# Performance work log

Measured on AMD Instinct MI355X. Metric: run time of the kernel, lower is better.

The kernel has to match this reference:

```python
import jax, jax.numpy as jnp
import numpy as np


def conv_block(x, w1, b1, w2, b2):
    # 1x1 convs == per-pixel channel matmuls. x: [b, C, H, W]
    h = jax.nn.relu(jnp.einsum('bchw,oc->bohw', x, w1) + b1[None, :, None, None])
    return jnp.einsum('bchw,oc->bohw', h, w2) + b2[None, :, None, None]


def setup_inputs() -> dict:
    key = jax.random.key(0)
    ks = jax.random.split(key, 9)
    C, Ck = 256, 256 // 8
    bs, H, W = 4, 64, 64
    s_in = 1.0 / np.sqrt(C)
    s_k = 1.0 / np.sqrt(Ck)
    F_input = jax.random.normal(ks[0], (bs, C, H, W), dtype=jnp.float32)
    return {
        'F_input': F_input,
        'w1a': jax.random.normal(ks[1], (Ck, C), dtype=jnp.float32) * s_in,
        'b1a': jax.random.normal(ks[2], (Ck,), dtype=jnp.float32) * s_in,
        'w1b': jax.random.normal(ks[3], (Ck, Ck), dtype=jnp.float32) * s_k,
        'b1b': jax.random.normal(ks[4], (Ck,), dtype=jnp.float32) * s_k,
        'w2a': jax.random.normal(ks[5], (Ck, C), dtype=jnp.float32) * s_in,
        'b2a': jax.random.normal(ks[6], (Ck,), dtype=jnp.float32) * s_in,
        'w2b': jax.random.normal(ks[7], (Ck, Ck), dtype=jnp.float32) * s_k,
        'b2b': jax.random.normal(ks[8], (Ck,), dtype=jnp.float32) * s_k,
    }


def reference(F_input, w1a, b1a, w1b, b1b, w2a, b2a, w2b, b2b):
    bs, C, H, W = F_input.shape
    N = H * W
    q = conv_block(F_input, w1a, b1a, w1b, b1b).reshape(bs, -1, N)  # [b, Ck, N]
    k = conv_block(F_input, w2a, b2a, w2b, b2b).reshape(bs, -1, N)  # [b, Ck, N]
    # mm_1[b, n, m] = sum_c q[b, c, n] * k[b, c, m]
    scores = jnp.einsum('bcn,bcm->bnm', q, k)  # [b, N, N]
    S = jax.nn.softmax(scores, axis=-1)
    Fr = F_input.reshape(bs, C, N)
    # bmm(F_reshape, S^T): out[b, c, n] = sum_m F[b, c, m] * S[b, n, m]
    mm2 = jnp.einsum('bcm,bnm->bcn', Fr, S).reshape(bs, C, H, W)
    return F_input + mm2
```

## Files before the change

### kernel.cpp

```cpp
#include <hip/hip_runtime.h>
#include <math.h>

typedef __attribute__((ext_vector_type(4))) float f32x4;
typedef __attribute__((ext_vector_type(8))) short bf16x8;
typedef __attribute__((ext_vector_type(4))) unsigned int uint4v;

#define LOG2E 1.4426950408889634f

static __device__ __forceinline__ unsigned short f2bf(float f) {
  union { float f; unsigned int i; } u; u.f = f;
  unsigned int r = u.i + 0x7fffu + ((u.i >> 16) & 1u);
  return (unsigned short)(r >> 16);
}

__global__ __launch_bounds__(256) void k_wprep(const float* __restrict__ w1a,
                                               const float* __restrict__ w2a,
                                               float* __restrict__ w1aT,
                                               float* __restrict__ w2aT) {
  int i = blockIdx.x * 256 + threadIdx.x;
  if (i < 32 * 256) {
    int o = i >> 8, c = i & 255;
    w1aT[c * 32 + o] = w1a[i];
    w2aT[c * 32 + o] = w2a[i];
  }
}

__global__ __launch_bounds__(256) void k_qk(
    const float* __restrict__ F,
    const float* __restrict__ w1aT, const float* __restrict__ b1a,
    const float* __restrict__ w1b,  const float* __restrict__ b1b,
    const float* __restrict__ w2aT, const float* __restrict__ b2a,
    const float* __restrict__ w2b,  const float* __restrict__ b2b,
    unsigned short* __restrict__ Fbf,
    unsigned short* __restrict__ qT,
    unsigned short* __restrict__ kT) {
  const int p = blockIdx.x >> 6;
  const int nflat = ((blockIdx.x & 63) << 8) | threadIdx.x;
  const int b = nflat >> 12, n = nflat & 4095;
  const float* __restrict__ wA = p ? w2aT : w1aT;
  const float* __restrict__ bA = p ? b2a : b1a;
  const float* __restrict__ wB = p ? w2b : w1b;
  const float* __restrict__ bB = p ? b2b : b1b;
  const float* Fb = F + ((size_t)b * 256) * 4096 + n;

  float h[32];
#pragma unroll
  for (int o = 0; o < 32; ++o) h[o] = 0.f;

  for (int c = 0; c < 256; ++c) {
    float f = Fb[(size_t)c * 4096];
    if (p == 0) Fbf[((size_t)b * 256 + c) * 4096 + n] = f2bf(f);
#pragma unroll
    for (int o = 0; o < 32; ++o) h[o] += wA[c * 32 + o] * f;
  }
#pragma unroll
  for (int o = 0; o < 32; ++o) h[o] = fmaxf(h[o] + bA[o], 0.f);

  unsigned int pack[16];
#pragma unroll
  for (int o2 = 0; o2 < 32; o2 += 2) {
    float s0 = bB[o2], s1 = bB[o2 + 1];
#pragma unroll
    for (int o = 0; o < 32; ++o) {
      s0 += wB[o2 * 32 + o] * h[o];
      s1 += wB[(o2 + 1) * 32 + o] * h[o];
    }
    if (p == 0) { s0 *= LOG2E; s1 *= LOG2E; }
    pack[o2 >> 1] = (unsigned int)f2bf(s0) | ((unsigned int)f2bf(s1) << 16);
  }
  unsigned short* dst = (p ? kT : qT) + (size_t)nflat * 32;
  uint4v* d4 = (uint4v*)dst;
#pragma unroll
  for (int i = 0; i < 4; ++i) {
    uint4v v = {pack[4 * i], pack[4 * i + 1], pack[4 * i + 2], pack[4 * i + 3]};
    d4[i] = v;
  }
}

__global__ __launch_bounds__(256, 1) void k_attn(
    const unsigned short* __restrict__ qT,
    const unsigned short* __restrict__ kT,
    const unsigned short* __restrict__ Fbf,
    const float* __restrict__ F,
    float* __restrict__ out) {
  __shared__ unsigned short Vt[256][72];
  __shared__ unsigned short Pb[4][16][72];

  const int tid = threadIdx.x;
  const int w = tid >> 6;
  const int lane = tid & 63;
  const int lo = lane & 15;
  const int hi = lane >> 4;

  const int bid = (int)blockIdx.x;
  const int swz = (bid & 7) * 32 + (bid >> 3);
  const int b = swz >> 6;
  const int n0 = (swz & 63) << 6;
  const int nw = n0 + (w << 4);

  const bf16x8 qfrag =
      *(const bf16x8*)(qT + ((size_t)(b << 12) + nw + lo) * 32 + hi * 8);
  const unsigned short* kTb = kT + ((size_t)(b << 12)) * 32;
  const unsigned short* Fb = Fbf + ((size_t)b << 20);

  f32x4 oacc[16];
#pragma unroll
  for (int i = 0; i < 16; ++i) oacc[i] = (f32x4){0.f, 0.f, 0.f, 0.f};
  float m2[4] = {-INFINITY, -INFINITY, -INFINITY, -INFINITY};
  float lr[4] = {0.f, 0.f, 0.f, 0.f};

  const int c0 = tid >> 3;
  const int ch = tid & 7;

  for (int mt = 0; mt < 64; ++mt) {
    {
      const unsigned short* src = Fb + (size_t)c0 * 4096 + (mt << 6) + (ch << 3);
#pragma unroll
      for (int pp = 0; pp < 8; ++pp) {
        bf16x8 v = *(const bf16x8*)(src + (size_t)(pp * 32) * 4096);
        *(bf16x8*)(&Vt[c0 + pp * 32][ch << 3]) = v;
      }
    }
    __syncthreads();

    f32x4 s[4];
#pragma unroll
    for (int mf = 0; mf < 4; ++mf) {
      bf16x8 kf = *(const bf16x8*)(kTb +
          ((size_t)((mt << 6) + (mf << 4) + lo)) * 32 + hi * 8);
      f32x4 z = (f32x4){0.f, 0.f, 0.f, 0.f};
      s[mf] = __builtin_amdgcn_mfma_f32_16x16x32_bf16(qfrag, kf, z, 0, 0, 0);
    }

    float scale[4];
#pragma unroll
    for (int r = 0; r < 4; ++r) {
      float t = fmaxf(fmaxf(s[0][r], s[1][r]), fmaxf(s[2][r], s[3][r]));
      t = fmaxf(t, __shfl_xor(t, 1));
      t = fmaxf(t, __shfl_xor(t, 2));
      t = fmaxf(t, __shfl_xor(t, 4));
      t = fmaxf(t, __shfl_xor(t, 8));
      float mnew = fmaxf(m2[r], t);
      scale[r] = exp2f(m2[r] - mnew);
      m2[r] = mnew;
    }

    float rsum[4] = {0.f, 0.f, 0.f, 0.f};
#pragma unroll
    for (int mf = 0; mf < 4; ++mf) {
#pragma unroll
      for (int r = 0; r < 4; ++r) {
        float p = exp2f(s[mf][r] - m2[r]);
        rsum[r] += p;
        Pb[w][(hi << 2) + r][(mf << 4) + lo] = f2bf(p);
      }
    }
#pragma unroll
    for (int r = 0; r < 4; ++r) {
      float t = rsum[r];
      t += __shfl_xor(t, 1);
      t += __shfl_xor(t, 2);
      t += __shfl_xor(t, 4);
      t += __shfl_xor(t, 8);
      lr[r] = lr[r] * scale[r] + t;
    }
#pragma unroll
    for (int cs = 0; cs < 16; ++cs) {
#pragma unroll
      for (int r = 0; r < 4; ++r) oacc[cs][r] *= scale[r];
    }

#pragma unroll
    for (int ms = 0; ms < 2; ++ms) {
      bf16x8 pf = *(const bf16x8*)(&Pb[w][lo][(ms << 5) + (hi << 3)]);
#pragma unroll
      for (int cs = 0; cs < 16; ++cs) {
        bf16x8 vf = *(const bf16x8*)(&Vt[(cs << 4) + lo][(ms << 5) + (hi << 3)]);
        oacc[cs] = __builtin_amdgcn_mfma_f32_16x16x32_bf16(pf, vf, oacc[cs], 0, 0, 0);
      }
    }
    __syncthreads();
  }

  float inv[4];
#pragma unroll
  for (int r = 0; r < 4; ++r) inv[r] = 1.f / lr[r];
#pragma unroll
  for (int cs = 0; cs < 16; ++cs) {
#pragma unroll
    for (int r = 0; r < 4; ++r) {
      size_t idx = ((size_t)(b * 256) + (cs << 4) + lo) * 4096 + nw + (hi << 2) + r;
      out[idx] = F[idx] + oacc[cs][r] * inv[r];
    }
  }
}

extern "C" void kernel_launch(void* const* d_in, const int* in_sizes, int n_in,
                              void* d_out, int out_size, void* d_ws, size_t ws_size,
                              hipStream_t stream) {
  const float* F   = (const float*)d_in[0];
  const float* w1a = (const float*)d_in[1];
  const float* b1a = (const float*)d_in[2];
  const float* w1b = (const float*)d_in[3];
  const float* b1b = (const float*)d_in[4];
  const float* w2a = (const float*)d_in[5];
  const float* b2a = (const float*)d_in[6];
  const float* w2b = (const float*)d_in[7];
  const float* b2b = (const float*)d_in[8];
  float* out = (float*)d_out;

  char* ws = (char*)d_ws;
  float* w1aT = (float*)(ws);
  float* w2aT = (float*)(ws + 32768);
  unsigned short* Fbf = (unsigned short*)(ws + 65536);
  unsigned short* qT  = (unsigned short*)(ws + 65536 + 8388608);
  unsigned short* kT  = (unsigned short*)(ws + 65536 + 8388608 + 1048576);

  hipLaunchKernelGGL(k_wprep, dim3(32), dim3(256), 0, stream, w1a, w2a, w1aT, w2aT);
  hipLaunchKernelGGL(k_qk, dim3(128), dim3(256), 0, stream,
                     F, w1aT, b1a, w1b, b1b, w2aT, b2a, w2b, b2b, Fbf, qT, kT);
  hipLaunchKernelGGL(k_attn, dim3(256), dim3(256), 0, stream, qT, kT, Fbf, F, out);
}
```

Baseline: 338.7 us.

## Pipeline attention with async LDS loads, split bf16 convert, rebalance QK kernel

The attention kernel is restructured. It now uses 32-key tiles and triple-buffered V tiles loaded with global_load_lds direct-to-LDS copies, plus XOR-swizzled LDS layouts. Each wave now owns 64 output channels for all 64 queries, with scale factors shared through LDS and rescaling skipped when every scale is 1. The bf16 conversion of F moves into its own vectorized kernel, and the QK projection kernel uses 128-thread blocks, twice the grid and register double-buffered F loads. The output epilogue uses vectorized float4 loads and stores. These changes aim to hide global latency and improve MFMA utilization, at the cost of an extra launch, more barriers per tile and higher LDS use.

```diff
diff --git a/kernel.cpp b/kernel.cpp
--- a/kernel.cpp
+++ b/kernel.cpp
@@ -3,14 +3,27 @@
 
 typedef __attribute__((ext_vector_type(4))) float f32x4;
 typedef __attribute__((ext_vector_type(8))) short bf16x8;
+typedef __attribute__((ext_vector_type(2))) unsigned int uint2v;
 typedef __attribute__((ext_vector_type(4))) unsigned int uint4v;
 
 #define LOG2E 1.4426950408889634f
+#define MT 32
+#define NIT 128
 
 static __device__ __forceinline__ unsigned short f2bf(float f) {
   union { float f; unsigned int i; } u; u.f = f;
   unsigned int r = u.i + 0x7fffu + ((u.i >> 16) & 1u);
   return (unsigned short)(r >> 16);
+}
+
+typedef __attribute__((address_space(3))) unsigned int lds_u32;
+typedef __attribute__((address_space(1))) unsigned int g_u32;
+
+static __device__ __forceinline__ void gload_lds16(const unsigned short* g,
+                                                   const unsigned short* l) {
+  __builtin_amdgcn_global_load_lds(
+      (const g_u32*)(unsigned long long)g,
+      (lds_u32*)(unsigned int)(unsigned long long)l, 16, 0, 0);
 }
 
 __global__ __launch_bounds__(256) void k_wprep(const float* __restrict__ w1a,
@@ -25,33 +38,59 @@
   }
 }
 
-__global__ __launch_bounds__(256) void k_qk(
+__global__ __launch_bounds__(256) void k_cvt(const float* __restrict__ F,
+                                             unsigned short* __restrict__ Fbf) {
+  size_t i = ((size_t)blockIdx.x * 256 + threadIdx.x) * 8;
+  f32x4 a = *(const f32x4*)(F + i);
+  f32x4 b = *(const f32x4*)(F + i + 4);
+  unsigned int u0 = (unsigned int)f2bf(a[0]) | ((unsigned int)f2bf(a[1]) << 16);
+  unsigned int u1 = (unsigned int)f2bf(a[2]) | ((unsigned int)f2bf(a[3]) << 16);
+  unsigned int u2 = (unsigned int)f2bf(b[0]) | ((unsigned int)f2bf(b[1]) << 16);
+  unsigned int u3 = (unsigned int)f2bf(b[2]) | ((unsigned int)f2bf(b[3]) << 16);
+  uint4v v = {u0, u1, u2, u3};
+  *(uint4v*)(Fbf + i) = v;
+}
+
+__global__ __launch_bounds__(128) void k_qk(
     const float* __restrict__ F,
     const float* __restrict__ w1aT, const float* __restrict__ b1a,
     const float* __restrict__ w1b,  const float* __restrict__ b1b,
     const float* __restrict__ w2aT, const float* __restrict__ b2a,
     const float* __restrict__ w2b,  const float* __restrict__ b2b,
-    unsigned short* __restrict__ Fbf,
     unsigned short* __restrict__ qT,
     unsigned short* __restrict__ kT) {
-  const int p = blockIdx.x >> 6;
-  const int nflat = ((blockIdx.x & 63) << 8) | threadIdx.x;
+  const int p = blockIdx.x & 1;
+  const int nflat = (blockIdx.x >> 1) * 128 + threadIdx.x;
   const int b = nflat >> 12, n = nflat & 4095;
-  const float* __restrict__ wA = p ? w2aT : w1aT;
-  const float* __restrict__ bA = p ? b2a : b1a;
-  const float* __restrict__ wB = p ? w2b : w1b;
-  const float* __restrict__ bB = p ? b2b : b1b;
-  const float* Fb = F + ((size_t)b * 256) * 4096 + n;
+  const float* wA = p ? w2aT : w1aT;
+  const float* bA = p ? b2a : b1a;
+  const float* wB = p ? w2b : w1b;
+  const float* bB = p ? b2b : b1b;
+  const float* Fp = F + ((size_t)b * 256) * 4096 + n;
 
   float h[32];
 #pragma unroll
   for (int o = 0; o < 32; ++o) h[o] = 0.f;
 
-  for (int c = 0; c < 256; ++c) {
-    float f = Fb[(size_t)c * 4096];
-    if (p == 0) Fbf[((size_t)b * 256 + c) * 4096 + n] = f2bf(f);
-#pragma unroll
-    for (int o = 0; o < 32; ++o) h[o] += wA[c * 32 + o] * f;
+  float fa[8], fb[8];
+#pragma unroll
+  for (int j = 0; j < 8; ++j) fa[j] = Fp[(size_t)j * 4096];
+
+  for (int cc = 0; cc < 256; cc += 16) {
+#pragma unroll
+    for (int j = 0; j < 8; ++j) fb[j] = Fp[(size_t)(cc + 8 + j) * 4096];
+#pragma unroll
+    for (int j = 0; j < 8; ++j)
+#pragma unroll
+      for (int o = 0; o < 32; ++o) h[o] += wA[(cc + j) * 32 + o] * fa[j];
+    if (cc + 16 < 256) {
+#pragma unroll
+      for (int j = 0; j < 8; ++j) fa[j] = Fp[(size_t)(cc + 16 + j) * 4096];
+    }
+#pragma unroll
+    for (int j = 0; j < 8; ++j)
+#pragma unroll
+      for (int o = 0; o < 32; ++o) h[o] += wA[(cc + 8 + j) * 32 + o] * fb[j];
   }
 #pragma unroll
   for (int o = 0; o < 32; ++o) h[o] = fmaxf(h[o] + bA[o], 0.f);
@@ -83,8 +122,10 @@
     const unsigned short* __restrict__ Fbf,
     const float* __restrict__ F,
     float* __restrict__ out) {
-  __shared__ unsigned short Vt[256][72];
-  __shared__ unsigned short Pb[4][16][72];
+  __shared__ unsigned short Vt[3][256 * MT];
+  __shared__ unsigned short Pb[2][64 * MT];
+  __shared__ float scl[2][64];
+  __shared__ float linv[64];
 
   const int tid = threadIdx.x;
   const int w = tid >> 6;
@@ -96,103 +137,133 @@
   const int swz = (bid & 7) * 32 + (bid >> 3);
   const int b = swz >> 6;
   const int n0 = (swz & 63) << 6;
-  const int nw = n0 + (w << 4);
-
-  const bf16x8 qfrag =
-      *(const bf16x8*)(qT + ((size_t)(b << 12) + nw + lo) * 32 + hi * 8);
+
+  const bf16x8 qfrag = *(const bf16x8*)(
+      qT + ((size_t)(b << 12) + n0 + (w << 4) + lo) * 32 + (hi << 3));
   const unsigned short* kTb = kT + ((size_t)(b << 12)) * 32;
   const unsigned short* Fb = Fbf + ((size_t)b << 20);
 
-  f32x4 oacc[16];
-#pragma unroll
-  for (int i = 0; i < 16; ++i) oacc[i] = (f32x4){0.f, 0.f, 0.f, 0.f};
-  float m2[4] = {-INFINITY, -INFINITY, -INFINITY, -INFINITY};
-  float lr[4] = {0.f, 0.f, 0.f, 0.f};
-
-  const int c0 = tid >> 3;
-  const int ch = tid & 7;
-
-  for (int mt = 0; mt < 64; ++mt) {
+  const int crow = lane >> 2;
+  const int pch = lane & 3;
+
+  f32x4 acc[4][4];
+#pragma unroll
+  for (int i = 0; i < 4; ++i)
+#pragma unroll
+    for (int j = 0; j < 4; ++j) acc[i][j] = (f32x4){0.f, 0.f, 0.f, 0.f};
+  float mrun = -INFINITY, lrun = 0.f;
+
+#pragma unroll
+  for (int i = 0; i < 4; ++i) {
+    int c = i * 64 + (w << 4) + crow;
+    gload_lds16(Fb + (size_t)c * 4096 + ((pch ^ (c & 3)) << 3),
+                &Vt[0][(i * 64 + (w << 4)) * MT]);
+  }
+  bf16x8 kc0 = *(const bf16x8*)(kTb + ((size_t)lo) * 32 + (hi << 3));
+  bf16x8 kc1 = *(const bf16x8*)(kTb + ((size_t)(16 + lo)) * 32 + (hi << 3));
+
+  int vb = 0, vn = 1;
+  for (int t = 0; t < NIT; ++t) {
+    if (t + 1 < NIT) {
+#pragma unroll
+      for (int i = 0; i < 4; ++i) {
+        int c = i * 64 + (w << 4) + crow;
+        gload_lds16(Fb + (size_t)c * 4096 + (size_t)(t + 1) * MT + ((pch ^ (c & 3)) << 3),
+                    &Vt[vn][(i * 64 + (w << 4)) * MT]);
+      }
+    }
+    bf16x8 kn0, kn1;
+    if (t + 1 < NIT) {
+      kn0 = *(const bf16x8*)(kTb + ((size_t)((t + 1) * MT) + lo) * 32 + (hi << 3));
+      kn1 = *(const bf16x8*)(kTb + ((size_t)((t + 1) * MT) + 16 + lo) * 32 + (hi << 3));
+    }
+    f32x4 z = (f32x4){0.f, 0.f, 0.f, 0.f};
+    f32x4 s0 = __builtin_amdgcn_mfma_f32_16x16x32_bf16(kc0, qfrag, z, 0, 0, 0);
+    f32x4 s1 = __builtin_amdgcn_mfma_f32_16x16x32_bf16(kc1, qfrag, z, 0, 0, 0);
+
+    float tmax = fmaxf(fmaxf(fmaxf(s0[0], s0[1]), fmaxf(s0[2], s0[3])),
+                       fmaxf(fmaxf(s1[0], s1[1]), fmaxf(s1[2], s1[3])));
+    tmax = fmaxf(tmax, __shfl_xor(tmax, 16));
+    tmax = fmaxf(tmax, __shfl_xor(tmax, 32));
+    float mnew = fmaxf(mrun, tmax);
+    float sc = exp2f(mrun - mnew);
+    mrun = mnew;
+    float p00 = exp2f(s0[0] - mnew), p01 = exp2f(s0[1] - mnew);
+    float p02 = exp2f(s0[2] - mnew), p03 = exp2f(s0[3] - mnew);
+    float p10 = exp2f(s1[0] - mnew), p11 = exp2f(s1[1] - mnew);
+    float p12 = exp2f(s1[2] - mnew), p13 = exp2f(s1[3] - mnew);
+    float rsum = p00 + p01 + p02 + p03 + p10 + p11 + p12 + p13;
+    rsum += __shfl_xor(rsum, 16);
+    rsum += __shfl_xor(rsum, 32);
+    lrun = lrun * sc + rsum;
+    if (hi == 0) scl[t & 1][(w << 4) + lo] = sc;
+
     {
-      const unsigned short* src = Fb + (size_t)c0 * 4096 + (mt << 6) + (ch << 3);
-#pragma unroll
-      for (int pp = 0; pp < 8; ++pp) {
-        bf16x8 v = *(const bf16x8*)(src + (size_t)(pp * 32) * 4096);
-        *(bf16x8*)(&Vt[c0 + pp * 32][ch << 3]) = v;
+      const int qr = (w << 4) + lo;
+      unsigned short* base = &Pb[t & 1][qr * MT];
+      int ch0 = (hi >> 1), ch1 = 2 + (hi >> 1);
+      uint2v v0 = {(unsigned int)f2bf(p00) | ((unsigned int)f2bf(p01) << 16),
+                   (unsigned int)f2bf(p02) | ((unsigned int)f2bf(p03) << 16)};
+      uint2v v1 = {(unsigned int)f2bf(p10) | ((unsigned int)f2bf(p11) << 16),
+                   (unsigned int)f2bf(p12) | ((unsigned int)f2bf(p13) << 16)};
+      *(uint2v*)(base + (((ch0 ^ (qr & 3)) << 3) | ((hi & 1) << 2))) = v0;
+      *(uint2v*)(base + (((ch1 ^ (qr & 3)) << 3) | ((hi & 1) << 2))) = v1;
+    }
+
+    __syncthreads();
+
+    {
+      f32x4 sv[4];
+      bool one = true;
+#pragma unroll
+      for (int qf = 0; qf < 4; ++qf) {
+        sv[qf] = *(const f32x4*)&scl[t & 1][(qf << 4) + (hi << 2)];
+        one = one && (sv[qf][0] == 1.f) && (sv[qf][1] == 1.f) &&
+              (sv[qf][2] == 1.f) && (sv[qf][3] == 1.f);
       }
-    }
-    __syncthreads();
-
-    f32x4 s[4];
-#pragma unroll
-    for (int mf = 0; mf < 4; ++mf) {
-      bf16x8 kf = *(const bf16x8*)(kTb +
-          ((size_t)((mt << 6) + (mf << 4) + lo)) * 32 + hi * 8);
-      f32x4 z = (f32x4){0.f, 0.f, 0.f, 0.f};
-      s[mf] = __builtin_amdgcn_mfma_f32_16x16x32_bf16(qfrag, kf, z, 0, 0, 0);
-    }
-
-    float scale[4];
-#pragma unroll
-    for (int r = 0; r < 4; ++r) {
-      float t = fmaxf(fmaxf(s[0][r], s[1][r]), fmaxf(s[2][r], s[3][r]));
-      t = fmaxf(t, __shfl_xor(t, 1));
-      t = fmaxf(t, __shfl_xor(t, 2));
-      t = fmaxf(t, __shfl_xor(t, 4));
-      t = fmaxf(t, __shfl_xor(t, 8));
-      float mnew = fmaxf(m2[r], t);
-      scale[r] = exp2f(m2[r] - mnew);
-      m2[r] = mnew;
-    }
-
-    float rsum[4] = {0.f, 0.f, 0.f, 0.f};
-#pragma unroll
-    for (int mf = 0; mf < 4; ++mf) {
-#pragma unroll
-      for (int r = 0; r < 4; ++r) {
-        float p = exp2f(s[mf][r] - m2[r]);
-        rsum[r] += p;
-        Pb[w][(hi << 2) + r][(mf << 4) + lo] = f2bf(p);
+      if (!__all(one)) {
+#pragma unroll
+        for (int qf = 0; qf < 4; ++qf)
+#pragma unroll
+          for (int cs = 0; cs < 4; ++cs) acc[qf][cs] *= sv[qf];
       }
     }
-#pragma unroll
-    for (int r = 0; r < 4; ++r) {
-      float t = rsum[r];
-      t += __shfl_xor(t, 1);
-      t += __shfl_xor(t, 2);
-      t += __shfl_xor(t, 4);
-      t += __shfl_xor(t, 8);
-      lr[r] = lr[r] * scale[r] + t;
-    }
-#pragma unroll
-    for (int cs = 0; cs < 16; ++cs) {
-#pragma unroll
-      for (int r = 0; r < 4; ++r) oacc[cs][r] *= scale[r];
-    }
-
-#pragma unroll
-    for (int ms = 0; ms < 2; ++ms) {
-      bf16x8 pf = *(const bf16x8*)(&Pb[w][lo][(ms << 5) + (hi << 3)]);
-#pragma unroll
-      for (int cs = 0; cs < 16; ++cs) {
-        bf16x8 vf = *(const bf16x8*)(&Vt[(cs << 4) + lo][(ms << 5) + (hi << 3)]);
-        oacc[cs] = __builtin_amdgcn_mfma_f32_16x16x32_bf16(pf, vf, oacc[cs], 0, 0, 0);
-      }
-    }
-    __syncthreads();
-  }
-
-  float inv[4];
-#pragma unroll
-  for (int r = 0; r < 4; ++r) inv[r] = 1.f / lr[r];
-#pragma unroll
-  for (int cs = 0; cs < 16; ++cs) {
-#pragma unroll
-    for (int r = 0; r < 4; ++r) {
-      size_t idx = ((size_t)(b * 256) + (cs << 4) + lo) * 4096 + nw + (hi << 2) + r;
-      out[idx] = F[idx] + oacc[cs][r] * inv[r];
-    }
-  }
+
+    bf16x8 pf[4], vf[4];
+#pragma unroll
+    for (int qf = 0; qf < 4; ++qf) {
+      int qr = (qf << 4) + lo;
+      pf[qf] = *(const bf16x8*)&Pb[t & 1][qr * MT + ((hi ^ (qr & 3)) << 3)];
+    }
+#pragma unroll
+    for (int cs = 0; cs < 4; ++cs) {
+      int c = (w << 6) + (cs << 4) + lo;
+      vf[cs] = *(const bf16x8*)&Vt[vb][c * MT + ((hi ^ (c & 3)) << 3)];
+    }
+#pragma unroll
+    for (int qf = 0; qf < 4; ++qf)
+#pragma unroll
+      for (int cs = 0; cs < 4; ++cs)
+        acc[qf][cs] = __builtin_amdgcn_mfma_f32_16x16x32_bf16(pf[qf], vf[cs], acc[qf][cs], 0, 0, 0);
+
+    kc0 = kn0; kc1 = kn1;
+    vb = vn; vn = (vn == 2) ? 0 : vn + 1;
+  }
+
+  if (hi == 0) linv[(w << 4) + lo] = 1.f / lrun;
+  __syncthreads();
+  f32x4 lv[4];
+#pragma unroll
+  for (int qf = 0; qf < 4; ++qf) lv[qf] = *(const f32x4*)&linv[(qf << 4) + (hi << 2)];
+#pragma unroll
+  for (int qf = 0; qf < 4; ++qf)
+#pragma unroll
+    for (int cs = 0; cs < 4; ++cs) {
+      size_t idx = ((size_t)(b * 256 + (w << 6) + (cs << 4) + lo)) * 4096 +
+                   n0 + (qf << 4) + (hi << 2);
+      f32x4 fv = *(const f32x4*)(F + idx);
+      *(f32x4*)(out + idx) = fv + acc[qf][cs] * lv[qf];
+    }
 }
 
 extern "C" void kernel_launch(void* const* d_in, const int* in_sizes, int n_in,
@@ -217,7 +288,8 @@
   unsigned short* kT  = (unsigned short*)(ws + 65536 + 8388608 + 1048576);
 
   hipLaunchKernelGGL(k_wprep, dim3(32), dim3(256), 0, stream, w1a, w2a, w1aT, w2aT);
-  hipLaunchKernelGGL(k_qk, dim3(128), dim3(256), 0, stream,
-                     F, w1aT, b1a, w1b, b1b, w2aT, b2a, w2b, b2b, Fbf, qT, kT);
+  hipLaunchKernelGGL(k_cvt, dim3(2048), dim3(256), 0, stream, F, Fbf);
+  hipLaunchKernelGGL(k_qk, dim3(256), dim3(128), 0, stream,
+                     F, w1aT, b1a, w1b, b1b, w2aT, b2a, w2b, b2b, qT, kT);
   hipLaunchKernelGGL(k_attn, dim3(256), dim3(256), 0, stream, qT, kT, Fbf, F, out);
 }
```

Result: no change. 342.7 us (+1.2%).

## Rewrite pipeline with MFMA projections, split-KV attention and combine kernel

Applied to the files above, without the earlier changes.

Replaces the scalar FP32 q/k projection with bf16 MFMA using hi/lo split weights, and adds a separate conversion kernel that writes F as bf16 in both layouts. The attention kernel switches to 32x32 MFMA tiles, reads V straight from global memory instead of LDS, and only rescales the accumulators when the running max grows by more than a threshold. It also splits the key range across up to 4 blocks (flash-decoding style) and adds a combine kernel to merge the partial results. These changes target low occupancy and poor parallelism with only 256 blocks, at the cost of extra partial-buffer traffic and additional kernel launches.

```diff
diff --git a/kernel.cpp b/kernel.cpp
--- a/kernel.cpp
+++ b/kernel.cpp
@@ -1,8 +1,11 @@
 #include <hip/hip_runtime.h>
+#include <hip/hip_bf16.h>
 #include <math.h>
 
 typedef __attribute__((ext_vector_type(4))) float f32x4;
+typedef __attribute__((ext_vector_type(16))) float f32x16;
 typedef __attribute__((ext_vector_type(8))) short bf16x8;
+typedef __attribute__((ext_vector_type(2))) unsigned int uint2v;
 typedef __attribute__((ext_vector_type(4))) unsigned int uint4v;
 
 #define LOG2E 1.4426950408889634f
@@ -12,186 +15,370 @@
   unsigned int r = u.i + 0x7fffu + ((u.i >> 16) & 1u);
   return (unsigned short)(r >> 16);
 }
-
-__global__ __launch_bounds__(256) void k_wprep(const float* __restrict__ w1a,
-                                               const float* __restrict__ w2a,
-                                               float* __restrict__ w1aT,
-                                               float* __restrict__ w2aT) {
+static __device__ __forceinline__ float bf2f(unsigned short s) {
+  union { unsigned int i; float f; } u; u.i = ((unsigned int)s) << 16;
+  return u.f;
+}
+static __device__ __forceinline__ unsigned int pkbf(float a, float b) {
+  return (unsigned int)f2bf(a) | ((unsigned int)f2bf(b) << 16);
+}
+static __device__ __forceinline__ bf16x8 mk8(uint2v a, uint2v b) {
+  union { unsigned int u[4]; bf16x8 v; } c;
+  c.u[0] = a[0]; c.u[1] = a[1]; c.u[2] = b[0]; c.u[3] = b[1];
+  return c.v;
+}
+static __device__ __forceinline__ f32x16 zero16() {
+  f32x16 z;
+#pragma unroll
+  for (int i = 0; i < 16; ++i) z[i] = 0.f;
+  return z;
+}
+
+__global__ __launch_bounds__(256) void k_wprep(
+    const float* __restrict__ w1a, const float* __restrict__ w2a,
+    const float* __restrict__ w1b, const float* __restrict__ w2b,
+    unsigned short* __restrict__ w1ah, unsigned short* __restrict__ w1al,
+    unsigned short* __restrict__ w2ah, unsigned short* __restrict__ w2al,
+    unsigned short* __restrict__ w1bh, unsigned short* __restrict__ w1bl,
+    unsigned short* __restrict__ w2bh, unsigned short* __restrict__ w2bl) {
   int i = blockIdx.x * 256 + threadIdx.x;
-  if (i < 32 * 256) {
-    int o = i >> 8, c = i & 255;
-    w1aT[c * 32 + o] = w1a[i];
-    w2aT[c * 32 + o] = w2a[i];
-  }
-}
-
-__global__ __launch_bounds__(256) void k_qk(
-    const float* __restrict__ F,
-    const float* __restrict__ w1aT, const float* __restrict__ b1a,
-    const float* __restrict__ w1b,  const float* __restrict__ b1b,
-    const float* __restrict__ w2aT, const float* __restrict__ b2a,
-    const float* __restrict__ w2b,  const float* __restrict__ b2b,
-    unsigned short* __restrict__ Fbf,
-    unsigned short* __restrict__ qT,
-    unsigned short* __restrict__ kT) {
-  const int p = blockIdx.x >> 6;
-  const int nflat = ((blockIdx.x & 63) << 8) | threadIdx.x;
-  const int b = nflat >> 12, n = nflat & 4095;
-  const float* __restrict__ wA = p ? w2aT : w1aT;
-  const float* __restrict__ bA = p ? b2a : b1a;
-  const float* __restrict__ wB = p ? w2b : w1b;
-  const float* __restrict__ bB = p ? b2b : b1b;
-  const float* Fb = F + ((size_t)b * 256) * 4096 + n;
-
-  float h[32];
-#pragma unroll
-  for (int o = 0; o < 32; ++o) h[o] = 0.f;
-
-  for (int c = 0; c < 256; ++c) {
-    float f = Fb[(size_t)c * 4096];
-    if (p == 0) Fbf[((size_t)b * 256 + c) * 4096 + n] = f2bf(f);
-#pragma unroll
-    for (int o = 0; o < 32; ++o) h[o] += wA[c * 32 + o] * f;
-  }
-#pragma unroll
-  for (int o = 0; o < 32; ++o) h[o] = fmaxf(h[o] + bA[o], 0.f);
-
-  unsigned int pack[16];
-#pragma unroll
-  for (int o2 = 0; o2 < 32; o2 += 2) {
-    float s0 = bB[o2], s1 = bB[o2 + 1];
-#pragma unroll
-    for (int o = 0; o < 32; ++o) {
-      s0 += wB[o2 * 32 + o] * h[o];
-      s1 += wB[(o2 + 1) * 32 + o] * h[o];
-    }
-    if (p == 0) { s0 *= LOG2E; s1 *= LOG2E; }
-    pack[o2 >> 1] = (unsigned int)f2bf(s0) | ((unsigned int)f2bf(s1) << 16);
-  }
-  unsigned short* dst = (p ? kT : qT) + (size_t)nflat * 32;
-  uint4v* d4 = (uint4v*)dst;
-#pragma unroll
-  for (int i = 0; i < 4; ++i) {
-    uint4v v = {pack[4 * i], pack[4 * i + 1], pack[4 * i + 2], pack[4 * i + 3]};
-    d4[i] = v;
-  }
-}
-
-__global__ __launch_bounds__(256, 1) void k_attn(
+  if (i < 8192) {
+    float a = w1a[i]; unsigned short h = f2bf(a);
+    w1ah[i] = h; w1al[i] = f2bf(a - bf2f(h));
+    float c = w2a[i]; h = f2bf(c);
+    w2ah[i] = h; w2al[i] = f2bf(c - bf2f(h));
+    if (i < 1024) {
+      float d = w1b[i]; h = f2bf(d);
+      w1bh[i] = h; w1bl[i] = f2bf(d - bf2f(h));
+      float e = w2b[i]; h = f2bf(e);
+      w2bh[i] = h; w2bl[i] = f2bf(e - bf2f(h));
+    }
+  }
+}
+
+__global__ __launch_bounds__(256) void k_cvt(const float* __restrict__ F,
+                                             unsigned short* __restrict__ Fbf,
+                                             unsigned short* __restrict__ FbfT) {
+  __shared__ unsigned short Lt[64][68];
+  const int bi = blockIdx.x;
+  const int b = bi >> 8, cg = (bi >> 6) & 3, ng = bi & 63;
+  const int tid = threadIdx.x;
+  {
+    const int cl = tid >> 2, part = tid & 3;
+    const size_t row = (size_t)(b * 256 + cg * 64 + cl);
+    const float* src = F + row * 4096 + ng * 64 + part * 16;
+    unsigned int pk[8];
+#pragma unroll
+    for (int i = 0; i < 4; ++i) {
+      f32x4 v = *(const f32x4*)(src + i * 4);
+      pk[2 * i]     = pkbf(v[0], v[1]);
+      pk[2 * i + 1] = pkbf(v[2], v[3]);
+    }
+    unsigned short* dst = Fbf + row * 4096 + ng * 64 + part * 16;
+    uint4v a = {pk[0], pk[1], pk[2], pk[3]};
+    uint4v c2 = {pk[4], pk[5], pk[6], pk[7]};
+    *(uint4v*)(dst) = a;
+    *(uint4v*)(dst + 8) = c2;
+    unsigned short* lrow = &Lt[cl][part * 16];
+#pragma unroll
+    for (int i = 0; i < 8; ++i) {
+      lrow[2 * i]     = (unsigned short)(pk[i] & 0xffffu);
+      lrow[2 * i + 1] = (unsigned short)(pk[i] >> 16);
+    }
+  }
+  __syncthreads();
+  {
+    const int nl = tid & 63, ch = tid >> 6;
+    unsigned short vals[16];
+#pragma unroll
+    for (int i = 0; i < 16; ++i) vals[i] = Lt[ch * 16 + i][nl];
+    unsigned int pk[8];
+#pragma unroll
+    for (int i = 0; i < 8; ++i)
+      pk[i] = (unsigned int)vals[2 * i] | ((unsigned int)vals[2 * i + 1] << 16);
+    unsigned short* dst = FbfT + ((size_t)(b * 4096 + ng * 64 + nl)) * 256 + cg * 64 + ch * 16;
+    uint4v v0 = {pk[0], pk[1], pk[2], pk[3]};
+    uint4v v1 = {pk[4], pk[5], pk[6], pk[7]};
+    *(uint4v*)(dst) = v0;
+    *(uint4v*)(dst + 8) = v1;
+  }
+}
+
+__global__ __launch_bounds__(256, 4) void k_qk(
+    const unsigned short* __restrict__ FbfT,
+    const unsigned short* __restrict__ w1ah, const unsigned short* __restrict__ w1al,
+    const unsigned short* __restrict__ w2ah, const unsigned short* __restrict__ w2al,
+    const unsigned short* __restrict__ w1bh, const unsigned short* __restrict__ w1bl,
+    const unsigned short* __restrict__ w2bh, const unsigned short* __restrict__ w2bl,
+    const float* __restrict__ b1a, const float* __restrict__ b1b,
+    const float* __restrict__ b2a, const float* __restrict__ b2b,
+    unsigned short* __restrict__ qT, unsigned short* __restrict__ kT) {
+  __shared__ unsigned short Hb[4][2][16][32];
+  const int tid = threadIdx.x;
+  const int w = tid >> 6, lane = tid & 63, lo = lane & 15, hi = lane >> 4;
+  const int p = blockIdx.x & 1;
+  const int nb = (blockIdx.x >> 1) * 64 + w * 16;
+  const unsigned short* wah = p ? w2ah : w1ah;
+  const unsigned short* wal = p ? w2al : w1al;
+  const unsigned short* wbh = p ? w2bh : w1bh;
+  const unsigned short* wbl = p ? w2bl : w1bl;
+  const float* bA = p ? b2a : b1a;
+  const float* bB = p ? b2b : b1b;
+  const int gq = (lo >> 1) & 7;
+
+  f32x4 acc[2];
+#pragma unroll
+  for (int m = 0; m < 2; ++m) acc[m] = (f32x4){0.f, 0.f, 0.f, 0.f};
+#pragma unroll
+  for (int ks = 0; ks < 8; ++ks) {
+    bf16x8 bf = *(const bf16x8*)(FbfT + (size_t)(nb + lo) * 256 + ks * 32 + hi * 8);
+#pragma unroll
+    for (int m = 0; m < 2; ++m) {
+      bf16x8 ah = *(const bf16x8*)(wah + (size_t)(m * 16 + lo) * 256 + ks * 32 + hi * 8);
+      bf16x8 al = *(const bf16x8*)(wal + (size_t)(m * 16 + lo) * 256 + ks * 32 + hi * 8);
+      acc[m] = __builtin_amdgcn_mfma_f32_16x16x32_bf16(ah, bf, acc[m], 0, 0, 0);
+      acc[m] = __builtin_amdgcn_mfma_f32_16x16x32_bf16(al, bf, acc[m], 0, 0, 0);
+    }
+  }
+#pragma unroll
+  for (int m = 0; m < 2; ++m) {
+    f32x4 bv = *(const f32x4*)(bA + m * 16 + hi * 4);
+    float hh[4], hl[4];
+#pragma unroll
+    for (int r = 0; r < 4; ++r) {
+      float h = fmaxf(acc[m][r] + bv[r], 0.f);
+      unsigned short s16 = f2bf(h);
+      hh[r] = bf2f(s16);
+      hl[r] = h - hh[r];
+    }
+    int c8 = (4 * m + hi) ^ gq;
+    uint2v vh = {pkbf(hh[0], hh[1]), pkbf(hh[2], hh[3])};
+    uint2v vl = {pkbf(hl[0], hl[1]), pkbf(hl[2], hl[3])};
+    *(uint2v*)&Hb[w][0][lo][c8 * 4] = vh;
+    *(uint2v*)&Hb[w][1][lo][c8 * 4] = vl;
+  }
+  bf16x8 hbf[2];
+#pragma unroll
+  for (int sp = 0; sp < 2; ++sp) {
+    uint2v ra = *(const uint2v*)&Hb[w][sp][lo][((2 * hi) ^ gq) * 4];
+    uint2v rb = *(const uint2v*)&Hb[w][sp][lo][((2 * hi + 1) ^ gq) * 4];
+    hbf[sp] = mk8(ra, rb);
+  }
+  f32x4 a2[2];
+#pragma unroll
+  for (int m = 0; m < 2; ++m) a2[m] = (f32x4){0.f, 0.f, 0.f, 0.f};
+#pragma unroll
+  for (int m = 0; m < 2; ++m) {
+    bf16x8 ah = *(const bf16x8*)(wbh + (size_t)(m * 16 + lo) * 32 + hi * 8);
+    bf16x8 al = *(const bf16x8*)(wbl + (size_t)(m * 16 + lo) * 32 + hi * 8);
+    a2[m] = __builtin_amdgcn_mfma_f32_16x16x32_bf16(ah, hbf[0], a2[m], 0, 0, 0);
+    a2[m] = __builtin_amdgcn_mfma_f32_16x16x32_bf16(ah, hbf[1], a2[m], 0, 0, 0);
+    a2[m] = __builtin_amdgcn_mfma_f32_16x16x32_bf16(al, hbf[0], a2[m], 0, 0, 0);
+  }
+  unsigned short* dst = (p ? kT : qT) + (size_t)(nb + lo) * 32;
+#pragma unroll
+  for (int m = 0; m < 2; ++m) {
+    f32x4 bv = *(const f32x4*)(bB + m * 16 + hi * 4);
+    float o[4];
+#pragma unroll
+    for (int r = 0; r < 4; ++r) {
+      o[r] = a2[m][r] + bv[r];
+      if (p == 0) o[r] *= LOG2E;
+    }
+    uint2v v = {pkbf(o[0], o[1]), pkbf(o[2], o[3])};
+    *(uint2v*)(dst + m * 16 + hi * 4) = v;
+  }
+}
+
+__global__ __launch_bounds__(256, 3) void k_attn(
     const unsigned short* __restrict__ qT,
     const unsigned short* __restrict__ kT,
     const unsigned short* __restrict__ Fbf,
     const float* __restrict__ F,
-    float* __restrict__ out) {
-  __shared__ unsigned short Vt[256][72];
-  __shared__ unsigned short Pb[4][16][72];
-
+    float* __restrict__ out,
+    float* __restrict__ Opart, float* __restrict__ Mpart, float* __restrict__ Lpart,
+    int spl, int tiles, int direct) {
+  __shared__ unsigned short PbA[4][1024];
+  __shared__ float sclA[4][64];
   const int tid = threadIdx.x;
-  const int w = tid >> 6;
-  const int lane = tid & 63;
-  const int lo = lane & 15;
-  const int hi = lane >> 4;
+  const int w = tid >> 6, lane = tid & 63, l31 = lane & 31, b5 = lane >> 5;
+  unsigned short* Pb = PbA[w];
+  float* scl = sclA[w];
+  const int g = (l31 >> 1) & 7;
 
   const int bid = (int)blockIdx.x;
-  const int swz = (bid & 7) * 32 + (bid >> 3);
-  const int b = swz >> 6;
-  const int n0 = (swz & 63) << 6;
-  const int nw = n0 + (w << 4);
-
-  const bf16x8 qfrag =
-      *(const bf16x8*)(qT + ((size_t)(b << 12) + nw + lo) * 32 + hi * 8);
+  int b, s, qt;
+  if (spl == 4)      { int gg = ((bid & 7) << 1) | (bid >> 9); b = gg >> 2; s = gg & 3; qt = (bid >> 3) & 63; }
+  else if (spl == 2) { int gg = bid & 7; b = gg >> 1; s = gg & 1; qt = bid >> 3; }
+  else               { int x = bid & 7; b = x >> 1; s = 0; qt = ((x & 1) << 5) | (bid >> 3); }
+
+  const unsigned short* qTb = qT + ((size_t)(b << 12) + qt * 64) * 32;
   const unsigned short* kTb = kT + ((size_t)(b << 12)) * 32;
-  const unsigned short* Fb = Fbf + ((size_t)b << 20);
-
-  f32x4 oacc[16];
-#pragma unroll
-  for (int i = 0; i < 16; ++i) oacc[i] = (f32x4){0.f, 0.f, 0.f, 0.f};
-  float m2[4] = {-INFINITY, -INFINITY, -INFINITY, -INFINITY};
-  float lr[4] = {0.f, 0.f, 0.f, 0.f};
-
-  const int c0 = tid >> 3;
-  const int ch = tid & 7;
-
-  for (int mt = 0; mt < 64; ++mt) {
-    {
-      const unsigned short* src = Fb + (size_t)c0 * 4096 + (mt << 6) + (ch << 3);
-#pragma unroll
-      for (int pp = 0; pp < 8; ++pp) {
-        bf16x8 v = *(const bf16x8*)(src + (size_t)(pp * 32) * 4096);
-        *(bf16x8*)(&Vt[c0 + pp * 32][ch << 3]) = v;
-      }
-    }
-    __syncthreads();
-
-    f32x4 s[4];
-#pragma unroll
-    for (int mf = 0; mf < 4; ++mf) {
-      bf16x8 kf = *(const bf16x8*)(kTb +
-          ((size_t)((mt << 6) + (mf << 4) + lo)) * 32 + hi * 8);
-      f32x4 z = (f32x4){0.f, 0.f, 0.f, 0.f};
-      s[mf] = __builtin_amdgcn_mfma_f32_16x16x32_bf16(qfrag, kf, z, 0, 0, 0);
-    }
-
-    float scale[4];
-#pragma unroll
-    for (int r = 0; r < 4; ++r) {
-      float t = fmaxf(fmaxf(s[0][r], s[1][r]), fmaxf(s[2][r], s[3][r]));
-      t = fmaxf(t, __shfl_xor(t, 1));
-      t = fmaxf(t, __shfl_xor(t, 2));
-      t = fmaxf(t, __shfl_xor(t, 4));
-      t = fmaxf(t, __shfl_xor(t, 8));
-      float mnew = fmaxf(m2[r], t);
-      scale[r] = exp2f(m2[r] - mnew);
-      m2[r] = mnew;
-    }
-
-    float rsum[4] = {0.f, 0.f, 0.f, 0.f};
-#pragma unroll
-    for (int mf = 0; mf < 4; ++mf) {
-#pragma unroll
-      for (int r = 0; r < 4; ++r) {
-        float p = exp2f(s[mf][r] - m2[r]);
-        rsum[r] += p;
-        Pb[w][(hi << 2) + r][(mf << 4) + lo] = f2bf(p);
-      }
-    }
-#pragma unroll
-    for (int r = 0; r < 4; ++r) {
-      float t = rsum[r];
-      t += __shfl_xor(t, 1);
-      t += __shfl_xor(t, 2);
-      t += __shfl_xor(t, 4);
-      t += __shfl_xor(t, 8);
-      lr[r] = lr[r] * scale[r] + t;
-    }
-#pragma unroll
-    for (int cs = 0; cs < 16; ++cs) {
-#pragma unroll
-      for (int r = 0; r < 4; ++r) oacc[cs][r] *= scale[r];
-    }
-
-#pragma unroll
-    for (int ms = 0; ms < 2; ++ms) {
-      bf16x8 pf = *(const bf16x8*)(&Pb[w][lo][(ms << 5) + (hi << 3)]);
-#pragma unroll
-      for (int cs = 0; cs < 16; ++cs) {
-        bf16x8 vf = *(const bf16x8*)(&Vt[(cs << 4) + lo][(ms << 5) + (hi << 3)]);
-        oacc[cs] = __builtin_amdgcn_mfma_f32_16x16x32_bf16(pf, vf, oacc[cs], 0, 0, 0);
-      }
-    }
-    __syncthreads();
-  }
-
-  float inv[4];
-#pragma unroll
-  for (int r = 0; r < 4; ++r) inv[r] = 1.f / lr[r];
-#pragma unroll
-  for (int cs = 0; cs < 16; ++cs) {
-#pragma unroll
-    for (int r = 0; r < 4; ++r) {
-      size_t idx = ((size_t)(b * 256) + (cs << 4) + lo) * 4096 + nw + (hi << 2) + r;
-      out[idx] = F[idx] + oacc[cs][r] * inv[r];
-    }
+  const unsigned short* Fb  = Fbf + ((size_t)b << 20);
+  const int cb = w << 6;
+  const int mt0 = s * tiles;
+
+  bf16x8 qf[2][2];
+#pragma unroll
+  for (int q2 = 0; q2 < 2; ++q2)
+#pragma unroll
+    for (int sl = 0; sl < 2; ++sl)
+      qf[q2][sl] = *(const bf16x8*)(qTb + (size_t)(q2 * 32 + l31) * 32 + sl * 16 + b5 * 8);
+
+  f32x16 acc[2][2];
+#pragma unroll
+  for (int i = 0; i < 2; ++i)
+#pragma unroll
+    for (int j = 0; j < 2; ++j) acc[i][j] = zero16();
+  float mrun[2] = {-INFINITY, -INFINITY};
+  float lrun[2] = {0.f, 0.f};
+
+  bf16x8 kc0 = *(const bf16x8*)(kTb + (size_t)((mt0 << 5) + l31) * 32 + b5 * 8);
+  bf16x8 kc1 = *(const bf16x8*)(kTb + (size_t)((mt0 << 5) + l31) * 32 + 16 + b5 * 8);
+
+  for (int t = 0; t < tiles; ++t) {
+    const int m0 = (mt0 + t) << 5;
+    bf16x8 vf[2][2];
+#pragma unroll
+    for (int ct = 0; ct < 2; ++ct)
+#pragma unroll
+      for (int sl = 0; sl < 2; ++sl)
+        vf[ct][sl] = *(const bf16x8*)(Fb + (size_t)(cb + ct * 32 + l31) * 4096 + m0 + sl * 16 + b5 * 8);
+    const int m1 = (t + 1 < tiles) ? (m0 + 32) : m0;
+    bf16x8 kn0 = *(const bf16x8*)(kTb + (size_t)(m1 + l31) * 32 + b5 * 8);
+    bf16x8 kn1 = *(const bf16x8*)(kTb + (size_t)(m1 + l31) * 32 + 16 + b5 * 8);
+
+#pragma unroll
+    for (int q2 = 0; q2 < 2; ++q2) {
+      f32x16 S = __builtin_amdgcn_mfma_f32_32x32x16_bf16(kc0, qf[q2][0], zero16(), 0, 0, 0);
+      S = __builtin_amdgcn_mfma_f32_32x32x16_bf16(kc1, qf[q2][1], S, 0, 0, 0);
+      float tmax = S[0];
+#pragma unroll
+      for (int i = 1; i < 16; ++i) tmax = fmaxf(tmax, S[i]);
+      tmax = fmaxf(tmax, __shfl_xor(tmax, 32));
+      if (__any(tmax - mrun[q2] > 8.f)) {
+        float mnew = fmaxf(mrun[q2], tmax);
+        float sc = exp2f(mrun[q2] - mnew);
+        mrun[q2] = mnew;
+        lrun[q2] *= sc;
+        scl[q2 * 32 + l31] = sc;
+#pragma unroll
+        for (int u = 0; u < 4; ++u) {
+          f32x4 sv = *(const f32x4*)&scl[q2 * 32 + u * 8 + b5 * 4];
+#pragma unroll
+          for (int r = 0; r < 4; ++r) {
+            acc[q2][0][u * 4 + r] *= sv[r];
+            acc[q2][1][u * 4 + r] *= sv[r];
+          }
+        }
+      }
+      float pv[16];
+      float rs = 0.f;
+#pragma unroll
+      for (int i = 0; i < 16; ++i) { pv[i] = exp2f(S[i] - mrun[q2]); rs += pv[i]; }
+      rs += __shfl_xor(rs, 32);
+      lrun[q2] += rs;
+#pragma unroll
+      for (int u = 0; u < 4; ++u) {
+        uint2v pw = {pkbf(pv[4 * u], pv[4 * u + 1]), pkbf(pv[4 * u + 2], pv[4 * u + 3])};
+        *(uint2v*)&Pb[l31 * 32 + (((2 * u + b5) ^ g) << 2)] = pw;
+      }
+      bf16x8 pa[2];
+#pragma unroll
+      for (int sl = 0; sl < 2; ++sl) {
+        uint2v ra = *(const uint2v*)&Pb[l31 * 32 + (((4 * sl + 2 * b5) ^ g) << 2)];
+        uint2v rb = *(const uint2v*)&Pb[l31 * 32 + (((4 * sl + 2 * b5 + 1) ^ g) << 2)];
+        pa[sl] = mk8(ra, rb);
+      }
+#pragma unroll
+      for (int ct = 0; ct < 2; ++ct) {
+        acc[q2][ct] = __builtin_amdgcn_mfma_f32_32x32x16_bf16(pa[0], vf[ct][0], acc[q2][ct], 0, 0, 0);
+        acc[q2][ct] = __builtin_amdgcn_mfma_f32_32x32x16_bf16(pa[1], vf[ct][1], acc[q2][ct], 0, 0, 0);
+      }
+    }
+    kc0 = kn0; kc1 = kn1;
+  }
+
+  if (direct) {
+#pragma unroll
+    for (int q2 = 0; q2 < 2; ++q2) scl[q2 * 32 + l31] = 1.f / lrun[q2];
+#pragma unroll
+    for (int q2 = 0; q2 < 2; ++q2)
+#pragma unroll
+      for (int ct = 0; ct < 2; ++ct) {
+        const int c = cb + ct * 32 + l31;
+#pragma unroll
+        for (int u = 0; u < 4; ++u) {
+          f32x4 lv = *(const f32x4*)&scl[q2 * 32 + u * 8 + b5 * 4];
+          size_t idx = ((size_t)(b * 256 + c)) * 4096 + qt * 64 + q2 * 32 + u * 8 + b5 * 4;
+          f32x4 fv = *(const f32x4*)(F + idx);
+          f32x4 o;
+#pragma unroll
+          for (int r = 0; r < 4; ++r) o[r] = fv[r] + acc[q2][ct][u * 4 + r] * lv[r];
+          *(f32x4*)(out + idx) = o;
+        }
+      }
+  } else {
+    const int bp = (b * spl + s) * 64 + qt;
+    if (w == 0 && b5 == 0) {
+#pragma unroll
+      for (int q2 = 0; q2 < 2; ++q2) {
+        Mpart[bp * 64 + q2 * 32 + l31] = mrun[q2];
+        Lpart[bp * 64 + q2 * 32 + l31] = lrun[q2];
+      }
+    }
+    float* Ob = Opart + (size_t)bp * 16384;
+#pragma unroll
+    for (int q2 = 0; q2 < 2; ++q2)
+#pragma unroll
+      for (int ct = 0; ct < 2; ++ct) {
+        const int c = cb + ct * 32 + l31;
+#pragma unroll
+        for (int u = 0; u < 4; ++u) {
+          f32x4 o;
+#pragma unroll
+          for (int r = 0; r < 4; ++r) o[r] = acc[q2][ct][u * 4 + r];
+          *(f32x4*)(Ob + (size_t)c * 64 + q2 * 32 + u * 8 + b5 * 4) = o;
+        }
+      }
+  }
+}
+
+__global__ __launch_bounds__(256) void k_comb(
+    const float* __restrict__ F, const float* __restrict__ Opart,
+    const float* __restrict__ Mpart, const float* __restrict__ Lpart,
+    float* __restrict__ out, int spl) {
+  const int bid = (int)blockIdx.x;
+  const int b = bid >> 6, qt = bid & 63;
+  const int tid = threadIdx.x, ql = tid & 63, cq = tid >> 6;
+  float mv[4], lv[4];
+  float M = -INFINITY;
+#pragma unroll
+  for (int s = 0; s < 4; ++s)
+    if (s < spl) {
+      int bp = (b * spl + s) * 64 + qt;
+      mv[s] = Mpart[bp * 64 + ql];
+      lv[s] = Lpart[bp * 64 + ql];
+      M = fmaxf(M, mv[s]);
+    }
+  float L = 0.f;
+#pragma unroll
+  for (int s = 0; s < 4; ++s)
+    if (s < spl) { mv[s] = exp2f(mv[s] - M); L += mv[s] * lv[s]; }
+  float Li = 1.f / L;
+  float a[4];
+#pragma unroll
+  for (int s = 0; s < 4; ++s) a[s] = (s < spl) ? mv[s] * Li : 0.f;
+
+  for (int cc = 0; cc < 64; ++cc) {
+    int c = cq * 64 + cc;
+    float accv = 0.f;
+#pragma unroll
+    for (int s = 0; s < 4; ++s)
+      if (s < spl)
+        accv += a[s] * Opart[((size_t)((b * spl + s) * 64 + qt)) * 16384 + c * 64 + ql];
+    size_t idx = ((size_t)(b * 256 + c)) * 4096 + qt * 64 + ql;
+    out[idx] = F[idx] + accv;
   }
 }
 
@@ -210,14 +397,40 @@
   float* out = (float*)d_out;
 
   char* ws = (char*)d_ws;
-  float* w1aT = (float*)(ws);
-  float* w2aT = (float*)(ws + 32768);
-  unsigned short* Fbf = (unsigned short*)(ws + 65536);
-  unsigned short* qT  = (unsigned short*)(ws + 65536 + 8388608);
-  unsigned short* kT  = (unsigned short*)(ws + 65536 + 8388608 + 1048576);
-
-  hipLaunchKernelGGL(k_wprep, dim3(32), dim3(256), 0, stream, w1a, w2a, w1aT, w2aT);
-  hipLaunchKernelGGL(k_qk, dim3(128), dim3(256), 0, stream,
-                     F, w1aT, b1a, w1b, b1b, w2aT, b2a, w2b, b2b, Fbf, qT, kT);
-  hipLaunchKernelGGL(k_attn, dim3(256), dim3(256), 0, stream, qT, kT, Fbf, F, out);
-}
+  unsigned short* qTw = (unsigned short*)(ws);
+  unsigned short* kTw = (unsigned short*)(ws + 1048576);
+  unsigned short* Fbf = (unsigned short*)(ws + 2097152);
+  const size_t obase = 10485760;
+  unsigned short* FbfT = (unsigned short*)(ws + obase);
+  char* wreg = ws + obase + 8388608;
+  unsigned short* w1ah = (unsigned short*)(wreg);
+  unsigned short* w1al = (unsigned short*)(wreg + 16384);
+  unsigned short* w2ah = (unsigned short*)(wreg + 32768);
+  unsigned short* w2al = (unsigned short*)(wreg + 49152);
+  unsigned short* w1bh = (unsigned short*)(wreg + 65536);
+  unsigned short* w1bl = (unsigned short*)(wreg + 67584);
+  unsigned short* w2bh = (unsigned short*)(wreg + 69632);
+  unsigned short* w2bl = (unsigned short*)(wreg + 71680);
+
+  int spl, direct = 0;
+  if (ws_size >= obase + 4ull * 16777216 + 8ull * 65536)      spl = 4;
+  else if (ws_size >= obase + 2ull * 16777216 + 4ull * 65536) spl = 2;
+  else { spl = 1; direct = 1; }
+
+  float* Opart = (float*)(ws + obase);
+  float* Mpart = (float*)(ws + obase + (size_t)spl * 16777216);
+  float* Lpart = (float*)(ws + obase + (size_t)spl * 16777216 + (size_t)spl * 65536);
+
+  hipLaunchKernelGGL(k_wprep, dim3(32), dim3(256), 0, stream,
+                     w1a, w2a, w1b, w2b,
+                     w1ah, w1al, w2ah, w2al, w1bh, w1bl, w2bh, w2bl);
+  hipLaunchKernelGGL(k_cvt, dim3(1024), dim3(256), 0, stream, F, Fbf, FbfT);
+  hipLaunchKernelGGL(k_qk, dim3(512), dim3(256), 0, stream,
+                     FbfT, w1ah, w1al, w2ah, w2al, w1bh, w1bl, w2bh, w2bl,
+                     b1a, b1b, b2a, b2b, qTw, kTw);
+  hipLaunchKernelGGL(k_attn, dim3(256 * spl), dim3(256), 0, stream,
+                     qTw, kTw, Fbf, F, out, Opart, Mpart, Lpart, spl, 128 / spl, direct);
+  if (!direct)
+    hipLaunchKernelGGL(k_comb, dim3(256), dim3(256), 0, stream,
+                       F, Opart, Mpart, Lpart, out, spl);
+}
```

Measured after the change: 318.2 us. 1.06x faster.
